# Kernel tuning notes

Measured on AMD Instinct MI355X. Metric: run time of the kernel, lower is better.

The kernel has to match this reference:

```python
import jax, jax.numpy as jnp
import numpy as np

N_NODES = 100000
D = 256
B = 64
EPG = 1024           # edges per query group in the last (pruned) layer
E1 = B * EPG         # 65536
E0 = 65536
K = 256              # max_edges


def setup_inputs() -> dict:
    key = jax.random.key(0)
    ks = jax.random.split(key, 20)
    # last-layer edges: sorted by eg_idx, exactly EPG edges per query group
    eg_idx1 = np.repeat(np.arange(B, dtype=np.int32), EPG)
    node_i1 = np.asarray(jax.random.randint(ks[0], (E1,), 0, N_NODES, dtype=jnp.int32))
    node_j1 = np.asarray(jax.random.randint(ks[1], (E1,), 0, N_NODES, dtype=jnp.int32))
    edges1 = np.zeros((E1, 8), dtype=np.int32)
    edges1[:, 0] = eg_idx1; edges1[:, 6] = node_i1; edges1[:, 7] = node_j1
    # earlier-layer edges (no pruning, any order)
    edges0 = np.zeros((E0, 8), dtype=np.int32)
    edges0[:, 0] = np.asarray(jax.random.randint(ks[2], (E0,), 0, B, dtype=jnp.int32))
    edges0[:, 6] = np.asarray(jax.random.randint(ks[3], (E0,), 0, N_NODES, dtype=jnp.int32))
    edges0[:, 7] = np.asarray(jax.random.randint(ks[4], (E0,), 0, N_NODES, dtype=jnp.int32))

    rn = lambda k, s, sc=1.0: (jax.random.normal(k, s, dtype=jnp.float32) * sc)
    return {
        "attended_nodes": jax.random.randint(ks[5], (B, 2), 0, N_NODES, dtype=jnp.int32),
        "node_score": jax.random.uniform(ks[6], (N_NODES,), dtype=jnp.float32),
        "edges0": jnp.asarray(edges0),
        "edges1": jnp.asarray(edges1),
        "rel_emb0": rn(ks[7], (E0, D)),
        "rel_emb1": rn(ks[8], (E1, D)),
        "memorized_embedding": rn(ks[9], (N_NODES, D)),
        "query_src_ts_emb": rn(ks[10], (B, D)),
        "query_rel_emb": rn(ks[11], (B, D)),
        "Wl": rn(ks[12], (4 * D, 2 * D), np.sqrt(2.0 / (4 * D))),
        "bl": rn(ks[13], (2 * D,), 0.01),
        "Wr": rn(ks[14], (4 * D, 2 * D), np.sqrt(2.0 / (4 * D))),
        "br": rn(ks[15], (2 * D,), 0.01),
        "Wc": rn(ks[16], (2 * D, 2 * D), np.sqrt(2.0 / (4 * D))),
        "bc": rn(ks[17], (2 * D,), 0.01),
        "Wlin": rn(ks[18], (D, D), np.sqrt(2.0 / D)),
        "blin": rn(ks[19], (D,), 0.01),
        "max_edges": K,
    }


def _g_score(hi, hj, rel, qs, qr, Wl, bl, Wr, br, Wc, bc):
    # bilinear MLP score: sum(LReLU(L @ Wl) * ((LReLU(R @ Wr)) @ Wc), -1)
    left = jnp.concatenate([hi, rel, qs, qr], axis=-1)   # [E, 4D]
    right = jnp.concatenate([hj, rel, qs, qr], axis=-1)  # [E, 4D]
    l = jax.nn.leaky_relu(left @ Wl + bl)                # [E, 2D]
    r = jax.nn.leaky_relu(right @ Wr + br) @ Wc + bc     # [E, 2D]
    return jnp.sum(l * r, axis=-1)                       # [E]


def _att_score(edges, emb, rel, qs_tab, qr_tab, Wl, bl, Wr, br, Wc, bc):
    hi = emb[edges[:, 6]]
    hj = emb[edges[:, 7]]
    qs = qs_tab[edges[:, 0]]
    qr = qr_tab[edges[:, 0]]
    return _g_score(hi, hj, rel, qs, qr, Wl, bl, Wr, br, Wc, bc)


def _segment_softmax(logits, seg, num_seg):
    m = jax.ops.segment_max(logits, seg, num_segments=num_seg)
    e = jnp.exp(logits - m[seg])
    s = jax.ops.segment_sum(e, seg, num_segments=num_seg)
    return e / s[seg]


def _update_nodes(edges, emb, logits):
    # aggregate source embeddings into targets, weighted by attention;
    # nodes with no incoming edge keep their old embedding.
    n = emb.shape[0]
    agg = jax.ops.segment_sum(logits[:, None] * emb[edges[:, 6]], edges[:, 7], num_segments=n)
    cnt = jax.ops.segment_sum(jnp.ones_like(logits), edges[:, 7], num_segments=n)
    return jnp.where((cnt > 0)[:, None], agg, emb)


def reference(attended_nodes, node_score, edges0, edges1, rel_emb0, rel_emb1,
              memorized_embedding, query_src_ts_emb, query_rel_emb,
              Wl, bl, Wr, br, Wc, bc, Wlin, blin, max_edges):
    n_nodes = memorized_embedding.shape[0]
    # ---- last layer: attention + segmented softmax over source node ----
    logits1 = _att_score(edges1, memorized_embedding, rel_emb1,
                         query_src_ts_emb, query_rel_emb, Wl, bl, Wr, br, Wc, bc)
    sm1 = _segment_softmax(logits1, edges1[:, 6], n_nodes)
    src_att = node_score[edges1[:, 6]]
    target_att = sm1 * src_att
    # ---- per-query top-k pruning (groups are contiguous, equal size EPG) ----
    b = B
    vals = target_att.reshape(b, EPG)
    pruned_att2, idx = jax.lax.top_k(vals, max_edges)              # [B, K]
    orig_indices = (jnp.arange(b, dtype=idx.dtype)[:, None] * EPG + idx).reshape(-1)
    pruned_att = pruned_att2.reshape(-1)                           # [B*K]
    pruned_edges = edges1[orig_indices]
    sm_pruned = sm1[orig_indices]
    # ---- node score aggregation ('sum') ----
    updated_node_score = jax.ops.segment_sum(sm_pruned * pruned_att,
                                             pruned_edges[:, 7], num_segments=n_nodes)
    # ---- propagate representations along pruned edges ----
    emb = _update_nodes(pruned_edges, memorized_embedding, sm_pruned)
    # ---- earlier layers (reversed) ----
    logits0 = _att_score(edges0, emb, rel_emb0, query_src_ts_emb, query_rel_emb,
                         Wl, bl, Wr, br, Wc, bc)
    sm0 = _segment_softmax(logits0, edges0[:, 6], n_nodes)
    emb = _update_nodes(edges0, emb, sm0)
    # ---- bypass: linear + LeakyReLU between steps ----
    emb = jax.nn.leaky_relu(emb @ Wlin + blin)
    return updated_node_score, emb, pruned_edges, orig_indices
```

## Files before the change

kernel.cpp:

```cpp
#include <hip/hip_runtime.h>
#include <math.h>


#define NNODES 100000
#define DDIM   256
#define NH     512
#define NGROUP 64
#define EPG    1024
#define E1N    65536
#define E0N    65536
#define KTOP   256

typedef __attribute__((ext_vector_type(8))) _Float16 h8v;
typedef __attribute__((ext_vector_type(4))) float f32x4;

__device__ __forceinline__ float lrelu(float x) { return x > 0.0f ? x : 0.01f * x; }

__device__ __forceinline__ unsigned fenc(float f) {
  unsigned u = __float_as_uint(f);
  return (u & 0x80000000u) ? ~u : (u | 0x80000000u);
}
__device__ __forceinline__ float fdec(unsigned k) {
  unsigned u = (k & 0x80000000u) ? (k & 0x7FFFFFFFu) : ~k;
  return __uint_as_float(u);
}

__device__ __forceinline__ void splitf(float v, unsigned short& h, unsigned short& l) {
  _Float16 hh = (_Float16)v;
  _Float16 ll = (_Float16)(v - (float)hh);
  h = __builtin_bit_cast(unsigned short, hh);
  l = __builtin_bit_cast(unsigned short, ll);
}

__device__ __forceinline__ f32x4 mfma16(h8v a, h8v b, f32x4 c) {
  return __builtin_amdgcn_mfma_f32_16x16x32_f16(a, b, c, 0, 0, 0);
}

__device__ __forceinline__ void pack8(uint4 a, uint4 b, uint4& ph, uint4& pl) {
  float v[8] = {__uint_as_float(a.x), __uint_as_float(a.y),
                __uint_as_float(a.z), __uint_as_float(a.w),
                __uint_as_float(b.x), __uint_as_float(b.y),
                __uint_as_float(b.z), __uint_as_float(b.w)};
  unsigned short h[8], l[8];
#pragma unroll
  for (int d = 0; d < 8; ++d) splitf(v[d], h[d], l[d]);
  ph = make_uint4((unsigned)h[0] | ((unsigned)h[1] << 16),
                  (unsigned)h[2] | ((unsigned)h[3] << 16),
                  (unsigned)h[4] | ((unsigned)h[5] << 16),
                  (unsigned)h[6] | ((unsigned)h[7] << 16));
  pl = make_uint4((unsigned)l[0] | ((unsigned)l[1] << 16),
                  (unsigned)l[2] | ((unsigned)l[3] << 16),
                  (unsigned)l[4] | ((unsigned)l[5] << 16),
                  (unsigned)l[6] | ((unsigned)l[7] << 16));
}

__global__ __launch_bounds__(512)
void qterm_kernel(const float* __restrict__ qse, const float* __restrict__ qre,
                  const float* __restrict__ Wl, const float* __restrict__ bl,
                  const float* __restrict__ Wr, const float* __restrict__ br,
                  float* __restrict__ qtl, float* __restrict__ qtr)
{
  const int g = blockIdx.x;
  const int o = threadIdx.x;
  __shared__ float sq[DDIM];
  __shared__ float sr[DDIM];
  if (o < DDIM) sq[o] = qse[(size_t)g * DDIM + o];
  else          sr[o - DDIM] = qre[(size_t)g * DDIM + (o - DDIM)];
  __syncthreads();
  float al = bl[o], ar = br[o];
  for (int k = 0; k < DDIM; ++k) {
    float a = sq[k], b = sr[k];
    al += a * Wl[(size_t)(512 + k) * NH + o] + b * Wl[(size_t)(768 + k) * NH + o];
    ar += a * Wr[(size_t)(512 + k) * NH + o] + b * Wr[(size_t)(768 + k) * NH + o];
  }
  qtl[(size_t)g * NH + o] = al;
  qtr[(size_t)g * NH + o] = ar;
}

__global__ __launch_bounds__(256)
void wprep_kernel(const float* __restrict__ Wl, const float* __restrict__ Wr,
                  const float* __restrict__ Wc,
                  unsigned short* __restrict__ WltH, unsigned short* __restrict__ WltL,
                  unsigned short* __restrict__ WrtH, unsigned short* __restrict__ WrtL,
                  unsigned short* __restrict__ WctH, unsigned short* __restrict__ WctL)
{
  __shared__ float shv[32][33];
  const int mtx = blockIdx.y;
  const int ti = blockIdx.x >> 4;
  const int tj = blockIdx.x & 15;
  const float* W = mtx == 0 ? Wl : (mtx == 1 ? Wr : Wc);
  unsigned short* OH = mtx == 0 ? WltH : (mtx == 1 ? WrtH : WctH);
  unsigned short* OL = mtx == 0 ? WltL : (mtx == 1 ? WrtL : WctL);
  const int t = threadIdx.x;
  const int r = t >> 3, c4 = (t & 7) * 4;
  *(float4*)&shv[r][c4] = *(const float4*)(W + (size_t)(ti * 32 + r) * 512 + tj * 32 + c4);
  __syncthreads();
  unsigned short h[4], l[4];
#pragma unroll
  for (int q = 0; q < 4; ++q) splitf(shv[c4 + q][r], h[q], l[q]);
  const size_t off = (size_t)(tj * 32 + r) * 512 + ti * 32 + c4;
  *(uint2*)(OH + off) = make_uint2((unsigned)h[0] | ((unsigned)h[1] << 16),
                                   (unsigned)h[2] | ((unsigned)h[3] << 16));
  *(uint2*)(OL + off) = make_uint2((unsigned)l[0] | ((unsigned)l[1] << 16),
                                   (unsigned)l[2] | ((unsigned)l[3] << 16));
}

__global__ __launch_bounds__(256)
void wlinprep_kernel(const float* __restrict__ Wlin, unsigned short* __restrict__ WlinT)
{
  __shared__ float shv[32][33];
  const int ti = blockIdx.x >> 3;
  const int tj = blockIdx.x & 7;
  const int t = threadIdx.x;
  const int r = t >> 3, c4 = (t & 7) * 4;
  *(float4*)&shv[r][c4] = *(const float4*)(Wlin + (size_t)(ti * 32 + r) * 256 + tj * 32 + c4);
  __syncthreads();
  unsigned short o[4];
#pragma unroll
  for (int q = 0; q < 4; ++q)
    o[q] = __builtin_bit_cast(unsigned short, (_Float16)shv[c4 + q][r]);
  *(uint2*)(WlinT + (size_t)(tj * 32 + r) * 256 + ti * 32 + c4) =
      make_uint2((unsigned)o[0] | ((unsigned)o[1] << 16),
                 (unsigned)o[2] | ((unsigned)o[3] << 16));
}

template<int SPLIT>
__global__ __launch_bounds__(512, 2)
void fused_score_kernel(const int* __restrict__ edges,
                        const float* __restrict__ emb,
                        const float* __restrict__ rel,
                        const unsigned short* __restrict__ BrH,
                        const unsigned short* __restrict__ BrL,
                        const unsigned short* __restrict__ BcH,
                        const unsigned short* __restrict__ BcL,
                        const unsigned short* __restrict__ BlH,
                        const unsigned short* __restrict__ BlL,
                        const float* __restrict__ qtr,
                        const float* __restrict__ qtl,
                        const float* __restrict__ bcv,
                        float* __restrict__ logits,
                        unsigned* __restrict__ mkey)
{
  constexpr int NP = SPLIT ? 2 : 1;
  __shared__ uint4 planesv[NP * 4096];
  __shared__ float red[8][64];
  __shared__ int sidxJ[64], sidxI[64], sgrp[64];

  const int tid  = threadIdx.x;
  const int lane = tid & 63;
  const int w    = tid >> 6;
  const int arow = lane & 15;
  const int grp  = lane >> 4;
  const int col0 = w * 64;
  const int rb   = blockIdx.x * 64;

  const int srow = tid >> 3;
  const int gs   = tid & 7;
  const int ssw  = srow & 7;

  if (tid < 64) {
    const int* er = edges + (size_t)(rb + tid) * 8;
    sgrp[tid]  = er[0];
    sidxI[tid] = er[6];
    sidxJ[tid] = er[7];
  }
  __syncthreads();

  const float* baseR = rel + (size_t)(rb + srow) * DDIM - 256;

  uint4 ai[16];
  {
    const float* bI = emb + (size_t)sidxI[srow] * DDIM;
#pragma unroll
    for (int q = 0; q < 8; ++q) {
      const int kf = q * 64 + ((gs ^ ssw) << 3);
      const float* s = (q < 4) ? (bI + kf) : (baseR + kf);
      ai[2 * q]     = ((const uint4*)s)[0];
      ai[2 * q + 1] = ((const uint4*)s)[1];
    }
  }

  {
    const float* bJ = emb + (size_t)sidxJ[srow] * DDIM;
#pragma unroll
    for (int q = 0; q < 8; ++q) {
      const int kf = q * 64 + ((gs ^ ssw) << 3);
      const float* s = (q < 4) ? (bJ + kf) : (baseR + kf);
      uint4 f0 = ((const uint4*)s)[0];
      uint4 f1 = ((const uint4*)s)[1];
      uint4 ph, pl;
      pack8(f0, f1, ph, pl);
      planesv[srow * 64 + q * 8 + gs] = ph;
      if (SPLIT) planesv[4096 + srow * 64 + q * 8 + gs] = pl;
    }
  }
  __syncthreads();

  const unsigned short* hiP = (const unsigned short*)planesv;
  const unsigned short* loP = hiP + 4096 * 8;

  auto gemm = [&](const unsigned short* BH, const unsigned short* BL,
                  f32x4 (&acc)[4][4]) {
    for (int ks = 0; ks < 16; ++ks) {
      const int k0 = ks * 32 + grp * 8;
      h8v bh[4], bl[4];
#pragma unroll
      for (int nt = 0; nt < 4; ++nt) {
        const size_t boff = (size_t)(col0 + nt * 16 + arow) * 512 + k0;
        bh[nt] = *(const h8v*)(BH + boff);
        if (SPLIT) bl[nt] = *(const h8v*)(BL + boff);
      }
#pragma unroll
      for (int mt = 0; mt < 4; ++mt) {
        const int row = mt * 16 + arow;
        const int gh = (ks * 4 + grp) ^ (row & 7);
        h8v h = *(const h8v*)(hiP + row * 512 + gh * 8);
        h8v l;
        if (SPLIT) l = *(const h8v*)(loP + row * 512 + gh * 8);
#pragma unroll
        for (int nt = 0; nt < 4; ++nt) {
          acc[mt][nt] = mfma16(h, bh[nt], acc[mt][nt]);
          if (SPLIT) {
            acc[mt][nt] = mfma16(h, bl[nt], acc[mt][nt]);
            acc[mt][nt] = mfma16(l, bh[nt], acc[mt][nt]);
          }
        }
      }
    }
  };

  f32x4 a1[4][4];
#pragma unroll
  for (int a = 0; a < 4; ++a)
#pragma unroll
    for (int b = 0; b < 4; ++b) a1[a][b] = (f32x4)0.0f;
  gemm(BrH, BrL, a1);
  __syncthreads();

  {
    unsigned short* hiW = (unsigned short*)planesv;
    unsigned short* loW = hiW + 4096 * 8;
#pragma unroll
    for (int mt = 0; mt < 4; ++mt)
#pragma unroll
      for (int nt = 0; nt < 4; ++nt) {
        const int c = col0 + nt * 16 + arow;
#pragma unroll
        for (int reg = 0; reg < 4; ++reg) {
          const int row = mt * 16 + grp * 4 + reg;
          float v = lrelu(a1[mt][nt][reg] + qtr[(size_t)sgrp[row] * NH + c]);
          unsigned short h, l;
          splitf(v, h, l);
          const int off = row * 512 + (((c >> 3) ^ (row & 7)) << 3) + (c & 7);
          hiW[off] = h;
          if (SPLIT) loW[off] = l;
        }
      }
  }
  __syncthreads();

  f32x4 ro[4][4];
#pragma unroll
  for (int a = 0; a < 4; ++a)
#pragma unroll
    for (int b = 0; b < 4; ++b) ro[a][b] = (f32x4)0.0f;
  gemm(BcH, BcL, ro);
#pragma unroll
  for (int nt = 0; nt < 4; ++nt) {
    const float bcval = bcv[col0 + nt * 16 + arow];
#pragma unroll
    for (int mt = 0; mt < 4; ++mt)
#pragma unroll
      for (int reg = 0; reg < 4; ++reg) ro[mt][nt][reg] += bcval;
  }
  __syncthreads();

#pragma unroll
  for (int q = 0; q < 8; ++q) {
    uint4 ph, pl;
    pack8(ai[2 * q], ai[2 * q + 1], ph, pl);
    planesv[srow * 64 + q * 8 + gs] = ph;
    if (SPLIT) planesv[4096 + srow * 64 + q * 8 + gs] = pl;
  }
  __syncthreads();

  f32x4 a3[4][4];
#pragma unroll
  for (int a = 0; a < 4; ++a)
#pragma unroll
    for (int b = 0; b < 4; ++b) a3[a][b] = (f32x4)0.0f;
  gemm(BlH, BlL, a3);
#pragma unroll
  for (int mt = 0; mt < 4; ++mt) {
#pragma unroll
    for (int reg = 0; reg < 4; ++reg) {
      const int row = mt * 16 + grp * 4 + reg;
      const int g = sgrp[row];
      float s = 0.0f;
#pragma unroll
      for (int nt = 0; nt < 4; ++nt) {
        const int c = col0 + nt * 16 + arow;
        float v = lrelu(a3[mt][nt][reg] + qtl[(size_t)g * NH + c]);
        s += v * ro[mt][nt][reg];
      }
      s += __shfl_xor(s, 1); s += __shfl_xor(s, 2);
      s += __shfl_xor(s, 4); s += __shfl_xor(s, 8);
      if ((lane & 15) == 0) red[w][row] = s;
    }
  }
  __syncthreads();
  if (tid < 64) {
    float s = 0.0f;
#pragma unroll
    for (int p = 0; p < 8; ++p) s += red[p][tid];
    logits[rb + tid] = s;
    atomicMax(mkey + sidxI[tid], fenc(s));
  }
}

__global__ void smax_exp_kernel(const int* __restrict__ edges, const float* __restrict__ logits,
                                const unsigned* __restrict__ mkey, float* __restrict__ ssum,
                                float* __restrict__ sm, int* __restrict__ cnt, int E)
{
  int e = blockIdx.x * blockDim.x + threadIdx.x;
  if (e < E) {
    int s = edges[(size_t)e * 8 + 6];
    float ev = expf(logits[e] - fdec(mkey[s]));
    sm[e] = ev;
    atomicAdd(ssum + s, ev);
    if (cnt) atomicAdd(cnt + edges[(size_t)e * 8 + 7], 1);
  }
}

__global__ void smax_norm_kernel(const int* __restrict__ edges, const float* __restrict__ ssum,
                                 float* __restrict__ sm, const float* __restrict__ nscore,
                                 float* __restrict__ ta, int E)
{
  int e = blockIdx.x * blockDim.x + threadIdx.x;
  if (e < E) {
    int s = edges[(size_t)e * 8 + 6];
    float v = sm[e] / ssum[s];
    sm[e] = v;
    if (ta) ta[e] = v * nscore[s];
  }
}

__global__ __launch_bounds__(256)
void topk_kernel(const float* __restrict__ ta, const float* __restrict__ sm1,
                 const int* __restrict__ edges1,
                 float* __restrict__ out0, float* __restrict__ out2,
                 float* __restrict__ out3, float* __restrict__ smp,
                 int* __restrict__ prn_i, int* __restrict__ prn_j,
                 int* __restrict__ cnt1)
{
  __shared__ float v[EPG];
  __shared__ int   ix[EPG];
  const int g = blockIdx.x, tid = threadIdx.x;
  for (int t = tid; t < EPG; t += 256) { v[t] = ta[(size_t)g * EPG + t]; ix[t] = t; }
  __syncthreads();
  for (int k = 2; k <= EPG; k <<= 1) {
    for (int j = k >> 1; j > 0; j >>= 1) {
      for (int t = tid; t < EPG; t += 256) {
        int l = t ^ j;
        if (l > t) {
          float va = v[t], vb = v[l];
          int ia = ix[t], ib = ix[l];
          bool aFirst = (va > vb) || (va == vb && ia < ib);
          bool up = ((t & k) == 0);
          bool sw = up ? !aFirst : aFirst;
          if (sw) { v[t] = vb; ix[t] = ib; v[l] = va; ix[l] = ia; }
        }
      }
      __syncthreads();
    }
  }
  const int r = tid;
  const int oi = ix[r];
  const float val = v[r];
  const int orig = g * EPG + oi;
  out3[(size_t)g * KTOP + r] = (float)orig;
  const int* er = edges1 + (size_t)orig * 8;
#pragma unroll
  for (int c = 0; c < 8; ++c)
    out2[((size_t)(g * KTOP + r)) * 8 + c] = (float)er[c];
  const int ii = er[6], jj = er[7];
  const float smv = sm1[orig];
  smp[(size_t)g * KTOP + r] = smv;
  prn_i[(size_t)g * KTOP + r] = ii;
  prn_j[(size_t)g * KTOP + r] = jj;
  atomicAdd(out0 + jj, smv * val);
  atomicAdd(cnt1 + jj, 1);
}

__global__ void scatter_kernel(const int* __restrict__ idx_i, int si,
                               const int* __restrict__ idx_j, int sj,
                               const float* __restrict__ w,
                               const float* __restrict__ semb,
                               float* __restrict__ agg)
{
  const int e0 = blockIdx.x * 4;
  const int o = threadIdx.x;
#pragma unroll
  for (int q = 0; q < 4; ++q) {
    const int e = e0 + q;
    const int i = idx_i[(size_t)e * si];
    const int j = idx_j[(size_t)e * sj];
    atomicAdd(agg + (size_t)j * DDIM + o, w[e] * semb[(size_t)i * DDIM + o]);
  }
}

__global__ void combine_kernel(const float* __restrict__ mememb, const int* __restrict__ cnt,
                               float* __restrict__ agg)
{
  size_t id = (size_t)blockIdx.x * 256 + threadIdx.x;
  if (cnt[id >> 8] == 0) agg[id] = mememb[id];
}

__global__ __launch_bounds__(512)
void final_mfma_kernel(const float* __restrict__ emb1, const float* __restrict__ agg0,
                       const int* __restrict__ cnt0,
                       const unsigned short* __restrict__ WlinT,
                       const float* __restrict__ blin, float* __restrict__ out)
{
  __shared__ int scnt[128];
  const int tid  = threadIdx.x;
  const int lane = tid & 63;
  const int wid  = tid >> 6;
  const int wm = wid >> 2, wn = wid & 3;
  const int rb = blockIdx.x * 128;
  const int arow = lane & 15;
  const int kgrp = (lane >> 4) * 8;
  const int row0 = wm * 64;
  const int col0 = wn * 64;

  if (tid < 128) {
    int r = rb + tid;
    scnt[tid] = (r < NNODES) ? cnt0[(r < NNODES) ? r : 0] : 0;
  }
  __syncthreads();

  f32x4 acc[4][4];
#pragma unroll
  for (int a = 0; a < 4; ++a)
#pragma unroll
    for (int b = 0; b < 4; ++b) acc[a][b] = (f32x4)0.0f;

  for (int ks = 0; ks < 8; ++ks) {
    const int k0 = ks * 32 + kgrp;
    h8v ah[4], bh[4];
#pragma unroll
    for (int nt = 0; nt < 4; ++nt)
      bh[nt] = *(const h8v*)(WlinT + (size_t)(col0 + nt * 16 + arow) * 256 + k0);
#pragma unroll
    for (int mt = 0; mt < 4; ++mt) {
      const int rl = row0 + mt * 16 + arow;
      int r = rb + rl;
      int rc = (r < NNODES) ? r : (NNODES - 1);
      const float* base = (scnt[rl] > 0) ? agg0 : emb1;
      const float* src = base + (size_t)rc * DDIM + k0;
      float4 f0 = *(const float4*)src;
      float4 f1 = *(const float4*)(src + 4);
      float v[8] = {f0.x, f0.y, f0.z, f0.w, f1.x, f1.y, f1.z, f1.w};
      h8v h;
#pragma unroll
      for (int d = 0; d < 8; ++d) h[d] = (_Float16)v[d];
      ah[mt] = h;
    }
#pragma unroll
    for (int mt = 0; mt < 4; ++mt)
#pragma unroll
      for (int nt = 0; nt < 4; ++nt)
        acc[mt][nt] = mfma16(ah[mt], bh[nt], acc[mt][nt]);
  }

  float bl4[4];
#pragma unroll
  for (int nt = 0; nt < 4; ++nt) bl4[nt] = blin[col0 + nt * 16 + arow];

#pragma unroll
  for (int mt = 0; mt < 4; ++mt)
#pragma unroll
    for (int reg = 0; reg < 4; ++reg) {
      const int r = rb + row0 + mt * 16 + (lane >> 4) * 4 + reg;
      if (r < NNODES) {
#pragma unroll
        for (int nt = 0; nt < 4; ++nt) {
          const int c = col0 + nt * 16 + arow;
          out[(size_t)r * DDIM + c] = lrelu(acc[mt][nt][reg] + bl4[nt]);
        }
      }
    }
}

extern "C" void kernel_launch(void* const* d_in, const int* in_sizes, int n_in,
                              void* d_out, int out_size, void* d_ws, size_t ws_size,
                              hipStream_t stream)
{
  (void)in_sizes; (void)n_in; (void)out_size; (void)ws_size;

  const float* node_score = (const float*)d_in[1];
  const int*   edges0 = (const int*)d_in[2];
  const int*   edges1 = (const int*)d_in[3];
  const float* rel0   = (const float*)d_in[4];
  const float* rel1   = (const float*)d_in[5];
  const float* mememb = (const float*)d_in[6];
  const float* qse    = (const float*)d_in[7];
  const float* qre    = (const float*)d_in[8];
  const float* Wl     = (const float*)d_in[9];
  const float* bl     = (const float*)d_in[10];
  const float* Wr     = (const float*)d_in[11];
  const float* br     = (const float*)d_in[12];
  const float* Wc     = (const float*)d_in[13];
  const float* bc     = (const float*)d_in[14];
  const float* Wlin   = (const float*)d_in[15];
  const float* blin   = (const float*)d_in[16];

  float* out0 = (float*)d_out;
  float* out1 = out0 + NNODES;
  float* out2 = out1 + (size_t)NNODES * DDIM;
  float* out3 = out2 + (size_t)NGROUP * KTOP * 8;

  char* wptr = (char*)d_ws;
  auto alloc = [&](size_t bytes) -> char* {
    char* p = wptr;
    wptr += (bytes + 255) & ~(size_t)255;
    return p;
  };
  float*    qtl     = (float*)alloc((size_t)NGROUP * NH * 4);
  float*    qtr     = (float*)alloc((size_t)NGROUP * NH * 4);
  float*    logits1 = (float*)alloc((size_t)E1N * 4);
  float*    sm1     = (float*)alloc((size_t)E1N * 4);
  float*    ta      = (float*)alloc((size_t)E1N * 4);
  float*    logits0 = (float*)alloc((size_t)E0N * 4);
  float*    sm0     = (float*)alloc((size_t)E0N * 4);
  unsigned* mkey    = (unsigned*)alloc((size_t)NNODES * 4);
  float*    ssum    = (float*)alloc((size_t)NNODES * 4);
  int*      cnt1    = (int*)alloc((size_t)NNODES * 4);
  int*      cnt0    = (int*)alloc((size_t)NNODES * 4);
  float*    smp     = (float*)alloc((size_t)NGROUP * KTOP * 4);
  int*      prn_i   = (int*)alloc((size_t)NGROUP * KTOP * 4);
  int*      prn_j   = (int*)alloc((size_t)NGROUP * KTOP * 4);
  float*    agg1    = (float*)alloc((size_t)NNODES * DDIM * 4);

  unsigned short* WltH = (unsigned short*)alloc((size_t)512 * 512 * 2);
  unsigned short* WltL = (unsigned short*)alloc((size_t)512 * 512 * 2);
  unsigned short* WrtH = (unsigned short*)alloc((size_t)512 * 512 * 2);
  unsigned short* WrtL = (unsigned short*)alloc((size_t)512 * 512 * 2);
  unsigned short* WctH = (unsigned short*)alloc((size_t)512 * 512 * 2);
  unsigned short* WctL = (unsigned short*)alloc((size_t)512 * 512 * 2);
  unsigned short* WlnT = (unsigned short*)alloc((size_t)256 * 256 * 2);

  (void)hipMemsetAsync(agg1, 0, (size_t)NNODES * DDIM * 4, stream);
  (void)hipMemsetAsync(cnt1, 0, (size_t)NNODES * 4, stream);
  (void)hipMemsetAsync(mkey, 0, (size_t)NNODES * 4, stream);
  (void)hipMemsetAsync(ssum, 0, (size_t)NNODES * 4, stream);
  (void)hipMemsetAsync(out0, 0, (size_t)NNODES * 4, stream);

  qterm_kernel<<<NGROUP, 512, 0, stream>>>(qse, qre, Wl, bl, Wr, br, qtl, qtr);
  {
    dim3 g(256, 3);
    wprep_kernel<<<g, 256, 0, stream>>>(Wl, Wr, Wc, WltH, WltL, WrtH, WrtL, WctH, WctL);
  }
  wlinprep_kernel<<<64, 256, 0, stream>>>(Wlin, WlnT);

  fused_score_kernel<1><<<E1N / 64, 512, 0, stream>>>(
      edges1, mememb, rel1, WrtH, WrtL, WctH, WctL, WltH, WltL,
      qtr, qtl, bc, logits1, mkey);

  smax_exp_kernel<<<E1N / 256, 256, 0, stream>>>(edges1, logits1, mkey, ssum, sm1,
                                                 nullptr, E1N);
  smax_norm_kernel<<<E1N / 256, 256, 0, stream>>>(edges1, ssum, sm1, node_score, ta, E1N);
  topk_kernel<<<NGROUP, 256, 0, stream>>>(ta, sm1, edges1, out0, out2, out3,
                                          smp, prn_i, prn_j, cnt1);
  scatter_kernel<<<NGROUP * KTOP / 4, 256, 0, stream>>>(prn_i, 1, prn_j, 1, smp,
                                                        mememb, agg1);
  combine_kernel<<<NNODES, 256, 0, stream>>>(mememb, cnt1, agg1);

  (void)hipMemsetAsync(mkey, 0, (size_t)NNODES * 4, stream);
  (void)hipMemsetAsync(ssum, 0, (size_t)NNODES * 4, stream);
  (void)hipMemsetAsync(cnt0, 0, (size_t)NNODES * 4, stream);
  (void)hipMemsetAsync(out1, 0, (size_t)NNODES * DDIM * 4, stream);

  fused_score_kernel<0><<<E0N / 64, 512, 0, stream>>>(
      edges0, agg1, rel0, WrtH, WrtL, WctH, WctL, WltH, WltL,
      qtr, qtl, bc, logits0, mkey);

  smax_exp_kernel<<<E0N / 256, 256, 0, stream>>>(edges0, logits0, mkey, ssum, sm0,
                                                 cnt0, E0N);
  smax_norm_kernel<<<E0N / 256, 256, 0, stream>>>(edges0, ssum, sm0, nullptr, nullptr, E0N);
  scatter_kernel<<<E0N / 4, 256, 0, stream>>>(edges0 + 6, 8, edges0 + 7, 8, sm0,
                                              agg1, out1);
  final_mfma_kernel<<<(NNODES + 127) / 128, 512, 0, stream>>>(agg1, out1, cnt0,
                                                              WlnT, blin, out1);
}
```

Measured before the change: 1.051 ms.

## Drop combine pass and layer-0 softmax normalize by selecting embedding source per row

Removes combine_kernel, which copied memorized embeddings into agg1 for nodes with no incoming pruned edges, a full 100000x256 pass. Consumers (fused score, scatter, final GEMM) now choose per row between agg1 and the memorized embedding using cnt1. It also fuses the layer-0 softmax normalization into the scatter, dividing by ssum inline, so smax_norm_kernel no longer runs for layer 0. The cost is extra per-row count lookups and branching in several kernels, and the final kernel now reads cnt1 and picks among three sources. The fused score kernel's swizzled load indexing is also rewritten.

```diff
diff --git a/kernel.cpp b/kernel.cpp
--- a/kernel.cpp
+++ b/kernel.cpp
@@ -127,7 +127,9 @@
 template<int SPLIT>
 __global__ __launch_bounds__(512, 2)
 void fused_score_kernel(const int* __restrict__ edges,
-                        const float* __restrict__ emb,
+                        const float* __restrict__ embA,
+                        const float* __restrict__ embB,
+                        const int* __restrict__ cntSel,
                         const float* __restrict__ rel,
                         const unsigned short* __restrict__ BrH,
                         const unsigned short* __restrict__ BrL,
@@ -141,8 +143,8 @@
                         float* __restrict__ logits,
                         unsigned* __restrict__ mkey)
 {
-  constexpr int NP = SPLIT ? 2 : 1;
-  __shared__ uint4 planesv[NP * 4096];
+  constexpr int NG = 4096;
+  __shared__ uint4 planesv[(SPLIT ? 2 : 1) * NG];
   __shared__ float red[8][64];
   __shared__ int sidxJ[64], sidxI[64], sgrp[64];
 
@@ -168,36 +170,44 @@
 
   const float* baseR = rel + (size_t)(rb + srow) * DDIM - 256;
 
+  auto rowbase = [&](int idx) -> const float* {
+    const float* b = (cntSel && cntSel[idx] > 0) ? embA : embB;
+    return b + (size_t)idx * DDIM;
+  };
+
   uint4 ai[16];
   {
-    const float* bI = emb + (size_t)sidxI[srow] * DDIM;
+    const float* bI = rowbase(sidxI[srow]);
 #pragma unroll
     for (int q = 0; q < 8; ++q) {
-      const int kf = q * 64 + ((gs ^ ssw) << 3);
-      const float* s = (q < 4) ? (bI + kf) : (baseR + kf);
+      const int lg = (q * 8 + gs) ^ ssw;
+      const int kf = lg << 3;
+      const float* s = (lg < 32) ? (bI + kf) : (baseR + kf);
       ai[2 * q]     = ((const uint4*)s)[0];
       ai[2 * q + 1] = ((const uint4*)s)[1];
     }
   }
 
   {
-    const float* bJ = emb + (size_t)sidxJ[srow] * DDIM;
+    const float* bJ = rowbase(sidxJ[srow]);
 #pragma unroll
     for (int q = 0; q < 8; ++q) {
-      const int kf = q * 64 + ((gs ^ ssw) << 3);
-      const float* s = (q < 4) ? (bJ + kf) : (baseR + kf);
+      const int g  = q * 8 + gs;
+      const int lg = g ^ ssw;
+      const int kf = lg << 3;
+      const float* s = (lg < 32) ? (bJ + kf) : (baseR + kf);
       uint4 f0 = ((const uint4*)s)[0];
       uint4 f1 = ((const uint4*)s)[1];
       uint4 ph, pl;
       pack8(f0, f1, ph, pl);
-      planesv[srow * 64 + q * 8 + gs] = ph;
-      if (SPLIT) planesv[4096 + srow * 64 + q * 8 + gs] = pl;
+      planesv[srow * 64 + g] = ph;
+      if (SPLIT) planesv[NG + srow * 64 + g] = pl;
     }
   }
   __syncthreads();
 
   const unsigned short* hiP = (const unsigned short*)planesv;
-  const unsigned short* loP = hiP + 4096 * 8;
+  const unsigned short* loP = hiP + (size_t)NG * 8;
 
   auto gemm = [&](const unsigned short* BH, const unsigned short* BL,
                   f32x4 (&acc)[4][4]) {
@@ -239,7 +249,7 @@
 
   {
     unsigned short* hiW = (unsigned short*)planesv;
-    unsigned short* loW = hiW + 4096 * 8;
+    unsigned short* loW = hiW + (size_t)NG * 8;
 #pragma unroll
     for (int mt = 0; mt < 4; ++mt)
 #pragma unroll
@@ -280,7 +290,7 @@
     uint4 ph, pl;
     pack8(ai[2 * q], ai[2 * q + 1], ph, pl);
     planesv[srow * 64 + q * 8 + gs] = ph;
-    if (SPLIT) planesv[4096 + srow * 64 + q * 8 + gs] = pl;
+    if (SPLIT) planesv[NG + srow * 64 + q * 8 + gs] = pl;
   }
   __syncthreads();
 
@@ -392,8 +402,8 @@
   atomicAdd(cnt1 + jj, 1);
 }
 
-__global__ void scatter_kernel(const int* __restrict__ idx_i, int si,
-                               const int* __restrict__ idx_j, int sj,
+__global__ void scatter_kernel(const int* __restrict__ idx_i,
+                               const int* __restrict__ idx_j,
                                const float* __restrict__ w,
                                const float* __restrict__ semb,
                                float* __restrict__ agg)
@@ -403,26 +413,41 @@
 #pragma unroll
   for (int q = 0; q < 4; ++q) {
     const int e = e0 + q;
-    const int i = idx_i[(size_t)e * si];
-    const int j = idx_j[(size_t)e * sj];
+    const int i = idx_i[e];
+    const int j = idx_j[e];
     atomicAdd(agg + (size_t)j * DDIM + o, w[e] * semb[(size_t)i * DDIM + o]);
   }
 }
 
-__global__ void combine_kernel(const float* __restrict__ mememb, const int* __restrict__ cnt,
-                               float* __restrict__ agg)
-{
-  size_t id = (size_t)blockIdx.x * 256 + threadIdx.x;
-  if (cnt[id >> 8] == 0) agg[id] = mememb[id];
+__global__ void scatter0_kernel(const int* __restrict__ edges,
+                                const float* __restrict__ sm,
+                                const float* __restrict__ ssum,
+                                const float* __restrict__ agg1,
+                                const float* __restrict__ mememb,
+                                const int* __restrict__ cnt1,
+                                float* __restrict__ out)
+{
+  const int e0 = blockIdx.x * 4;
+  const int o = threadIdx.x;
+#pragma unroll
+  for (int q = 0; q < 4; ++q) {
+    const int e = e0 + q;
+    const int i = edges[(size_t)e * 8 + 6];
+    const int j = edges[(size_t)e * 8 + 7];
+    const float wv = sm[e] / ssum[i];
+    const float* src = ((cnt1[i] > 0) ? agg1 : mememb) + (size_t)i * DDIM;
+    atomicAdd(out + (size_t)j * DDIM + o, wv * src[o]);
+  }
 }
 
 __global__ __launch_bounds__(512)
-void final_mfma_kernel(const float* __restrict__ emb1, const float* __restrict__ agg0,
-                       const int* __restrict__ cnt0,
+void final_mfma_kernel(const float* __restrict__ agg1, const float* __restrict__ mememb,
+                       const int* __restrict__ cnt1,
+                       const float* __restrict__ agg0, const int* __restrict__ cnt0,
                        const unsigned short* __restrict__ WlinT,
                        const float* __restrict__ blin, float* __restrict__ out)
 {
-  __shared__ int scnt[128];
+  __shared__ int ssel[128];
   const int tid  = threadIdx.x;
   const int lane = tid & 63;
   const int wid  = tid >> 6;
@@ -435,7 +460,11 @@
 
   if (tid < 128) {
     int r = rb + tid;
-    scnt[tid] = (r < NNODES) ? cnt0[(r < NNODES) ? r : 0] : 0;
+    int rc = (r < NNODES) ? r : 0;
+    int s = 0;
+    if (cnt0[rc] > 0) s = 2;
+    else if (cnt1[rc] > 0) s = 1;
+    ssel[tid] = s;
   }
   __syncthreads();
 
@@ -456,7 +485,8 @@
       const int rl = row0 + mt * 16 + arow;
       int r = rb + rl;
       int rc = (r < NNODES) ? r : (NNODES - 1);
-      const float* base = (scnt[rl] > 0) ? agg0 : emb1;
+      const int sel = ssel[rl];
+      const float* base = (sel == 2) ? agg0 : ((sel == 1) ? agg1 : mememb);
       const float* src = base + (size_t)rc * DDIM + k0;
       float4 f0 = *(const float4*)src;
       float4 f1 = *(const float4*)(src + 4);
@@ -564,7 +594,8 @@
   wlinprep_kernel<<<64, 256, 0, stream>>>(Wlin, WlnT);
 
   fused_score_kernel<1><<<E1N / 64, 512, 0, stream>>>(
-      edges1, mememb, rel1, WrtH, WrtL, WctH, WctL, WltH, WltL,
+      edges1, mememb, mememb, nullptr, rel1,
+      WrtH, WrtL, WctH, WctL, WltH, WltL,
       qtr, qtl, bc, logits1, mkey);
 
   smax_exp_kernel<<<E1N / 256, 256, 0, stream>>>(edges1, logits1, mkey, ssum, sm1,
@@ -572,9 +603,8 @@
   smax_norm_kernel<<<E1N / 256, 256, 0, stream>>>(edges1, ssum, sm1, node_score, ta, E1N);
   topk_kernel<<<NGROUP, 256, 0, stream>>>(ta, sm1, edges1, out0, out2, out3,
                                           smp, prn_i, prn_j, cnt1);
-  scatter_kernel<<<NGROUP * KTOP / 4, 256, 0, stream>>>(prn_i, 1, prn_j, 1, smp,
+  scatter_kernel<<<NGROUP * KTOP / 4, 256, 0, stream>>>(prn_i, prn_j, smp,
                                                         mememb, agg1);
-  combine_kernel<<<NNODES, 256, 0, stream>>>(mememb, cnt1, agg1);
 
   (void)hipMemsetAsync(mkey, 0, (size_t)NNODES * 4, stream);
   (void)hipMemsetAsync(ssum, 0, (size_t)NNODES * 4, stream);
@@ -582,14 +612,15 @@
   (void)hipMemsetAsync(out1, 0, (size_t)NNODES * DDIM * 4, stream);
 
   fused_score_kernel<0><<<E0N / 64, 512, 0, stream>>>(
-      edges0, agg1, rel0, WrtH, WrtL, WctH, WctL, WltH, WltL,
+      edges0, agg1, mememb, cnt1, rel0,
+      WrtH, WrtL, WctH, WctL, WltH, WltL,
       qtr, qtl, bc, logits0, mkey);
 
   smax_exp_kernel<<<E0N / 256, 256, 0, stream>>>(edges0, logits0, mkey, ssum, sm0,
                                                  cnt0, E0N);
-  smax_norm_kernel<<<E0N / 256, 256, 0, stream>>>(edges0, ssum, sm0, nullptr, nullptr, E0N);
-  scatter_kernel<<<E0N / 4, 256, 0, stream>>>(edges0 + 6, 8, edges0 + 7, 8, sm0,
-                                              agg1, out1);
-  final_mfma_kernel<<<(NNODES + 127) / 128, 512, 0, stream>>>(agg1, out1, cnt0,
+  scatter0_kernel<<<E0N / 4, 256, 0, stream>>>(edges0, sm0, ssum, agg1, mememb,
+                                               cnt1, out1);
+  final_mfma_kernel<<<(NNODES + 127) / 128, 512, 0, stream>>>(agg1, mememb, cnt1,
+                                                              out1, cnt0,
                                                               WlnT, blin, out1);
 }
```

Measured after the change: 1.035 ms. No clear change (-1.5%).
